# Performance work log

Measured on AMD Instinct MI355X. Metric: run time of the kernel, lower is better.

## Reference

```python
import jax, jax.numpy as jnp
import numpy as np

N_QUBITS = 4
N_LAYERS = 2
BATCH = 524288


def _ry(theta):
    # RY(theta) = [[cos(t/2), -sin(t/2)], [sin(t/2), cos(t/2)]], shape [..., 2, 2]
    c = jnp.cos(theta / 2)
    s = jnp.sin(theta / 2)
    return jnp.stack([jnp.stack([c, -s], -1), jnp.stack([s, c], -1)], -2).astype(jnp.complex64)


def _rz(theta):
    # RZ(theta) = diag(exp(-i t/2), exp(i t/2))
    p = jnp.exp(-1j * theta / 2)
    pc = jnp.exp(1j * theta / 2)
    z = jnp.zeros_like(p)
    return jnp.stack([jnp.stack([p, z], -1), jnp.stack([z, pc], -1)], -2).astype(jnp.complex64)


def _apply_1q(state, gate, q):
    # state: [B,2,2,2,2] (axis 1+q is qubit q, wire 0 most significant as in default.qubit)
    # gate: [2,2] (shared) or [B,2,2] (per-sample)
    letters = list('abcd')
    t = letters[q]
    out = letters.copy()
    out[q] = 'z'
    if gate.ndim == 3:
        sub = f"Bz{t},B{''.join(letters)}->B{''.join(out)}"
    else:
        sub = f"z{t},B{''.join(letters)}->B{''.join(out)}"
    return jnp.einsum(sub, gate, state)


def _cnot(state, c, t):
    # flip target axis on the control=1 slice
    s0 = jnp.take(state, 0, axis=1 + c)
    s1 = jnp.take(state, 1, axis=1 + c)
    ta = 1 + t - (1 if t > c else 0)
    s1 = jnp.flip(s1, axis=ta)
    return jnp.stack([s0, s1], axis=1 + c)


def _circuit(x, weights):
    B = x.shape[0]
    state = jnp.zeros((B, 2, 2, 2, 2), jnp.complex64).at[:, 0, 0, 0, 0].set(1.0)
    ry_in = _ry(x)  # [B, 4, 2, 2], per-sample input encoding
    for q in range(N_QUBITS):
        state = _apply_1q(state, ry_in[:, q], q)
    for l in range(N_LAYERS):
        for q in range(N_QUBITS):
            state = _apply_1q(state, _rz(weights[l, q, 0]), q)
            state = _apply_1q(state, _ry(weights[l, q, 1]), q)
        for q in range(N_QUBITS - 1):
            state = _cnot(state, q, q + 1)
        state = _cnot(state, N_QUBITS - 1, 0)
    probs = jnp.abs(state.reshape(B, 16)) ** 2
    # <Z_i> = sum_s p(s) * (1 - 2*bit_i(s)); wire 0 is the most significant bit
    bits = (np.arange(16)[:, None] >> np.arange(N_QUBITS - 1, -1, -1)) & 1
    signs = jnp.asarray(1.0 - 2.0 * bits, jnp.float32)  # [16, 4]
    return probs @ signs  # [B, 4]


def setup_inputs() -> dict:
    key = jax.random.key(0)
    k1, k2 = jax.random.split(key)
    x = jax.random.normal(k1, (BATCH, N_QUBITS), dtype=jnp.float32)
    # TorchLayer default init: uniform in [0, 2*pi)
    weights = jax.random.uniform(k2, (N_LAYERS, N_QUBITS, 2), dtype=jnp.float32, minval=0.0, maxval=2 * np.pi)
    return {"x": x, "weights": weights}


def reference(x, weights):
    return _circuit(x, weights)
```

## Files before the change

kernel.cpp:

```cpp
#include <hip/hip_runtime.h>

#define BATCH 524288
#define TPB 256
#define V 2

__global__ void qprep_kernel(const float* __restrict__ w, float* __restrict__ ws) {
    const int tid = threadIdx.x;
    if (tid >= 16) return;

    float stx[16], sty[16];
    #pragma unroll
    for (int i = 0; i < 16; i++) { stx[i] = 0.f; sty[i] = 0.f; }
    stx[tid] = 1.f;

    #pragma unroll
    for (int l = 0; l < 2; l++) {
        #pragma unroll
        for (int q = 0; q < 4; q++) {
            float cz, sz, cy, sy;
            __sincosf(0.5f * w[l * 8 + q * 2 + 0], &sz, &cz);
            __sincosf(0.5f * w[l * 8 + q * 2 + 1], &sy, &cy);
            const int mask = 8 >> q;
            #pragma unroll
            for (int i = 0; i < 16; i++) {
                float ax = stx[i], ay = sty[i];
                if (i & mask) { stx[i] = ax * cz - ay * sz; sty[i] = ay * cz + ax * sz; }
                else          { stx[i] = ax * cz + ay * sz; sty[i] = ay * cz - ax * sz; }
            }
            #pragma unroll
            for (int i = 0; i < 16; i++) {
                if (!(i & mask)) {
                    float a0x = stx[i], a0y = sty[i];
                    float a1x = stx[i | mask], a1y = sty[i | mask];
                    stx[i]        = cy * a0x - sy * a1x;
                    sty[i]        = cy * a0y - sy * a1y;
                    stx[i | mask] = sy * a0x + cy * a1x;
                    sty[i | mask] = sy * a0y + cy * a1y;
                }
            }
        }
        #pragma unroll
        for (int e = 0; e < 4; e++) {
            const int cqs[4] = {0, 1, 2, 3};
            const int tqs[4] = {1, 2, 3, 0};
            const int cm = 8 >> cqs[e];
            const int tm = 8 >> tqs[e];
            #pragma unroll
            for (int i = 0; i < 16; i++) {
                if ((i & cm) && !(i & tm)) {
                    float t0x = stx[i], t0y = sty[i];
                    stx[i] = stx[i | tm]; sty[i] = sty[i | tm];
                    stx[i | tm] = t0x;    sty[i | tm] = t0y;
                }
            }
        }
    }
    #pragma unroll
    for (int j = 0; j < 16; j++) {
        ws[j * 32 + tid]      = stx[j];
        ws[j * 32 + 16 + tid] = sty[j];
    }
}

__global__ __launch_bounds__(TPB, 4) void qmain_kernel(const float* __restrict__ x,
                                                       const float* __restrict__ U,
                                                       float* __restrict__ out) {
    const int base = blockIdx.x * (TPB * V) + threadIdx.x;

    float sv[V][16];
    #pragma unroll
    for (int v = 0; v < V; v++) {
        const int smp = base + v * TPB;
        const float4 xv = reinterpret_cast<const float4*>(x)[smp];
        float c0, s0, c1, s1, c2, s2, c3, s3;
        __sincosf(0.5f * xv.x, &s0, &c0);
        __sincosf(0.5f * xv.y, &s1, &c1);
        __sincosf(0.5f * xv.z, &s2, &c2);
        __sincosf(0.5f * xv.w, &s3, &c3);
        const float p01[4] = {c0 * c1, c0 * s1, s0 * c1, s0 * s1};
        const float p23[4] = {c2 * c3, c2 * s3, s2 * c3, s2 * s3};
        #pragma unroll
        for (int i = 0; i < 16; i++) sv[v][i] = p01[i >> 2] * p23[i & 3];
    }

    float z[V][4];
    #pragma unroll
    for (int v = 0; v < V; v++)
        #pragma unroll
        for (int i = 0; i < 4; i++) z[v][i] = 0.f;

    #pragma unroll
    for (int j = 0; j < 16; j++) {
        float re[V], im[V];
        #pragma unroll
        for (int v = 0; v < V; v++) { re[v] = 0.f; im[v] = 0.f; }
        #pragma unroll
        for (int k = 0; k < 16; k++) {
            const float ur = U[j * 32 + k];
            const float ui = U[j * 32 + 16 + k];
            #pragma unroll
            for (int v = 0; v < V; v++) {
                re[v] = fmaf(ur, sv[v][k], re[v]);
                im[v] = fmaf(ui, sv[v][k], im[v]);
            }
        }
        #pragma unroll
        for (int v = 0; v < V; v++) {
            const float p = re[v] * re[v] + im[v] * im[v];
            z[v][0] += (j & 8) ? -p : p;
            z[v][1] += (j & 4) ? -p : p;
            z[v][2] += (j & 2) ? -p : p;
            z[v][3] += (j & 1) ? -p : p;
        }
    }

    #pragma unroll
    for (int v = 0; v < V; v++) {
        const int smp = base + v * TPB;
        reinterpret_cast<float4*>(out)[smp] = make_float4(z[v][0], z[v][1], z[v][2], z[v][3]);
    }
}

extern "C" void kernel_launch(void* const* d_in, const int* in_sizes, int n_in,
                              void* d_out, int out_size, void* d_ws, size_t ws_size,
                              hipStream_t stream) {
    const float* x = (const float*)d_in[0];
    const float* w = (const float*)d_in[1];
    float* out = (float*)d_out;
    float* U = (float*)d_ws;

    qprep_kernel<<<1, 64, 0, stream>>>(w, U);
    const int grid = BATCH / (TPB * V);
    qmain_kernel<<<grid, TPB, 0, stream>>>(x, U, out);
}
```

Before: 68.79 us.

## Fuse unitary prep into main kernel via shared memory and skip basis state zero

The separate single-thread-block prep kernel is removed. Each block now rebuilds the 16x16 circuit unitary in shared memory with 16 threads, then synchronises before the batch work. The main loop reads unitary rows as float4 from LDS instead of global memory. Because the state is normalised, it skips basis state 0 and derives each <Z_i> as 1-2*sum of probabilities with bit i set. This cuts one kernel launch and one sixteenth of the matvec work, but every block now repeats the prep serially, and the result relies on the norm being exactly 1.

```diff
diff --git a/kernel.cpp b/kernel.cpp
--- a/kernel.cpp
+++ b/kernel.cpp
@@ -4,68 +4,69 @@
 #define TPB 256
 #define V 2
 
-__global__ void qprep_kernel(const float* __restrict__ w, float* __restrict__ ws) {
+__global__ __launch_bounds__(TPB, 4) void qfused_kernel(const float* __restrict__ x,
+                                                        const float* __restrict__ w,
+                                                        float* __restrict__ out) {
+    __shared__ __align__(16) float Ush[512];
     const int tid = threadIdx.x;
-    if (tid >= 16) return;
 
-    float stx[16], sty[16];
-    #pragma unroll
-    for (int i = 0; i < 16; i++) { stx[i] = 0.f; sty[i] = 0.f; }
-    stx[tid] = 1.f;
+    if (tid < 16) {
+        float stx[16], sty[16];
+        #pragma unroll
+        for (int i = 0; i < 16; i++) { stx[i] = 0.f; sty[i] = 0.f; }
+        stx[tid] = 1.f;
 
-    #pragma unroll
-    for (int l = 0; l < 2; l++) {
         #pragma unroll
-        for (int q = 0; q < 4; q++) {
-            float cz, sz, cy, sy;
-            __sincosf(0.5f * w[l * 8 + q * 2 + 0], &sz, &cz);
-            __sincosf(0.5f * w[l * 8 + q * 2 + 1], &sy, &cy);
-            const int mask = 8 >> q;
+        for (int l = 0; l < 2; l++) {
             #pragma unroll
-            for (int i = 0; i < 16; i++) {
-                float ax = stx[i], ay = sty[i];
-                if (i & mask) { stx[i] = ax * cz - ay * sz; sty[i] = ay * cz + ax * sz; }
-                else          { stx[i] = ax * cz + ay * sz; sty[i] = ay * cz - ax * sz; }
+            for (int q = 0; q < 4; q++) {
+                float cz, sz, cy, sy;
+                __sincosf(0.5f * w[l * 8 + q * 2 + 0], &sz, &cz);
+                __sincosf(0.5f * w[l * 8 + q * 2 + 1], &sy, &cy);
+                const int mask = 8 >> q;
+                #pragma unroll
+                for (int i = 0; i < 16; i++) {
+                    float ax = stx[i], ay = sty[i];
+                    if (i & mask) { stx[i] = ax * cz - ay * sz; sty[i] = ay * cz + ax * sz; }
+                    else          { stx[i] = ax * cz + ay * sz; sty[i] = ay * cz - ax * sz; }
+                }
+                #pragma unroll
+                for (int i = 0; i < 16; i++) {
+                    if (!(i & mask)) {
+                        float a0x = stx[i], a0y = sty[i];
+                        float a1x = stx[i | mask], a1y = sty[i | mask];
+                        stx[i]        = cy * a0x - sy * a1x;
+                        sty[i]        = cy * a0y - sy * a1y;
+                        stx[i | mask] = sy * a0x + cy * a1x;
+                        sty[i | mask] = sy * a0y + cy * a1y;
+                    }
+                }
             }
             #pragma unroll
-            for (int i = 0; i < 16; i++) {
-                if (!(i & mask)) {
-                    float a0x = stx[i], a0y = sty[i];
-                    float a1x = stx[i | mask], a1y = sty[i | mask];
-                    stx[i]        = cy * a0x - sy * a1x;
-                    sty[i]        = cy * a0y - sy * a1y;
-                    stx[i | mask] = sy * a0x + cy * a1x;
-                    sty[i | mask] = sy * a0y + cy * a1y;
+            for (int e = 0; e < 4; e++) {
+                const int cqs[4] = {0, 1, 2, 3};
+                const int tqs[4] = {1, 2, 3, 0};
+                const int cm = 8 >> cqs[e];
+                const int tm = 8 >> tqs[e];
+                #pragma unroll
+                for (int i = 0; i < 16; i++) {
+                    if ((i & cm) && !(i & tm)) {
+                        float t0x = stx[i], t0y = sty[i];
+                        stx[i] = stx[i | tm]; sty[i] = sty[i | tm];
+                        stx[i | tm] = t0x;    sty[i | tm] = t0y;
+                    }
                 }
             }
         }
         #pragma unroll
-        for (int e = 0; e < 4; e++) {
-            const int cqs[4] = {0, 1, 2, 3};
-            const int tqs[4] = {1, 2, 3, 0};
-            const int cm = 8 >> cqs[e];
-            const int tm = 8 >> tqs[e];
-            #pragma unroll
-            for (int i = 0; i < 16; i++) {
-                if ((i & cm) && !(i & tm)) {
-                    float t0x = stx[i], t0y = sty[i];
-                    stx[i] = stx[i | tm]; sty[i] = sty[i | tm];
-                    stx[i | tm] = t0x;    sty[i | tm] = t0y;
-                }
-            }
+        for (int j = 0; j < 16; j++) {
+            Ush[j * 32 + tid]      = stx[j];
+            Ush[j * 32 + 16 + tid] = sty[j];
         }
     }
-    #pragma unroll
-    for (int j = 0; j < 16; j++) {
-        ws[j * 32 + tid]      = stx[j];
-        ws[j * 32 + 16 + tid] = sty[j];
-    }
-}
+    __syncthreads();
 
-__global__ __launch_bounds__(TPB, 4) void qmain_kernel(const float* __restrict__ x,
-                                                       const float* __restrict__ U,
-                                                       float* __restrict__ out) {
-    const int base = blockIdx.x * (TPB * V) + threadIdx.x;
+    const int base = blockIdx.x * (TPB * V) + tid;
 
     float sv[V][16];
     #pragma unroll
@@ -83,41 +84,44 @@
         for (int i = 0; i < 16; i++) sv[v][i] = p01[i >> 2] * p23[i & 3];
     }
 
-    float z[V][4];
+    float acc[V][4];
     #pragma unroll
     for (int v = 0; v < V; v++)
         #pragma unroll
-        for (int i = 0; i < 4; i++) z[v][i] = 0.f;
+        for (int i = 0; i < 4; i++) acc[v][i] = 0.f;
 
     #pragma unroll
-    for (int j = 0; j < 16; j++) {
-        float re[V], im[V];
+    for (int j = 1; j < 16; j++) {
+        float ur[16], ui[16];
         #pragma unroll
-        for (int v = 0; v < V; v++) { re[v] = 0.f; im[v] = 0.f; }
-        #pragma unroll
-        for (int k = 0; k < 16; k++) {
-            const float ur = U[j * 32 + k];
-            const float ui = U[j * 32 + 16 + k];
-            #pragma unroll
-            for (int v = 0; v < V; v++) {
-                re[v] = fmaf(ur, sv[v][k], re[v]);
-                im[v] = fmaf(ui, sv[v][k], im[v]);
-            }
+        for (int t = 0; t < 4; t++) {
+            const float4 a = reinterpret_cast<const float4*>(Ush + j * 32)[t];
+            ur[4 * t + 0] = a.x; ur[4 * t + 1] = a.y; ur[4 * t + 2] = a.z; ur[4 * t + 3] = a.w;
+            const float4 b = reinterpret_cast<const float4*>(Ush + j * 32 + 16)[t];
+            ui[4 * t + 0] = b.x; ui[4 * t + 1] = b.y; ui[4 * t + 2] = b.z; ui[4 * t + 3] = b.w;
         }
         #pragma unroll
         for (int v = 0; v < V; v++) {
-            const float p = re[v] * re[v] + im[v] * im[v];
-            z[v][0] += (j & 8) ? -p : p;
-            z[v][1] += (j & 4) ? -p : p;
-            z[v][2] += (j & 2) ? -p : p;
-            z[v][3] += (j & 1) ? -p : p;
+            float re = 0.f, im = 0.f;
+            #pragma unroll
+            for (int k = 0; k < 16; k++) {
+                re = fmaf(ur[k], sv[v][k], re);
+                im = fmaf(ui[k], sv[v][k], im);
+            }
+            const float p = fmaf(re, re, im * im);
+            if (j & 8) acc[v][0] += p;
+            if (j & 4) acc[v][1] += p;
+            if (j & 2) acc[v][2] += p;
+            if (j & 1) acc[v][3] += p;
         }
     }
 
     #pragma unroll
     for (int v = 0; v < V; v++) {
         const int smp = base + v * TPB;
-        reinterpret_cast<float4*>(out)[smp] = make_float4(z[v][0], z[v][1], z[v][2], z[v][3]);
+        reinterpret_cast<float4*>(out)[smp] =
+            make_float4(fmaf(-2.f, acc[v][0], 1.f), fmaf(-2.f, acc[v][1], 1.f),
+                        fmaf(-2.f, acc[v][2], 1.f), fmaf(-2.f, acc[v][3], 1.f));
     }
 }
 
@@ -127,9 +131,6 @@
     const float* x = (const float*)d_in[0];
     const float* w = (const float*)d_in[1];
     float* out = (float*)d_out;
-    float* U = (float*)d_ws;
-
-    qprep_kernel<<<1, 64, 0, stream>>>(w, U);
     const int grid = BATCH / (TPB * V);
-    qmain_kernel<<<grid, TPB, 0, stream>>>(x, U, out);
+    qfused_kernel<<<grid, TPB, 0, stream>>>(x, w, out);
 }
```

Result: slower. 94.41 us (+37.2%).

## Compute circuit unitary product with split-fp16 MFMA instead of scalar FMAs

Applied to the files above, without the earlier changes.

The per-sample 16x16 complex unitary times real state vector is moved onto MFMA 16x16x32 f16 instructions. Both the unitary and the state are split into high and low fp16 parts to recover near-fp32 accuracy. The state vectors are staged through swizzled shared memory, and the Z expectations are reduced with cross-lane shuffles. One sample per thread replaces two, which adds an LDS round trip and a block barrier in exchange for removing the large scalar FMA count.

```diff
diff --git a/kernel.cpp b/kernel.cpp
--- a/kernel.cpp
+++ b/kernel.cpp
@@ -2,7 +2,9 @@
 
 #define BATCH 524288
 #define TPB 256
-#define V 2
+
+typedef _Float16 half8 __attribute__((ext_vector_type(8)));
+typedef float f32x4 __attribute__((ext_vector_type(4)));
 
 __global__ void qprep_kernel(const float* __restrict__ w, float* __restrict__ ws) {
     const int tid = threadIdx.x;
@@ -65,59 +67,93 @@
 __global__ __launch_bounds__(TPB, 4) void qmain_kernel(const float* __restrict__ x,
                                                        const float* __restrict__ U,
                                                        float* __restrict__ out) {
-    const int base = blockIdx.x * (TPB * V) + threadIdx.x;
+    __shared__ __align__(16) _Float16 Sb[TPB * 32];
 
-    float sv[V][16];
+    const int tid  = threadIdx.x;
+    const int lane = tid & 63;
+    const int wave = tid >> 6;
+    const int l15  = lane & 15;
+    const int lg   = lane >> 4;
+
+    const int k8 = (lg & 1) * 8;
+    const float* urow = U + l15 * 32 + k8;
+    const float4 r0 = *reinterpret_cast<const float4*>(urow);
+    const float4 r1 = *reinterpret_cast<const float4*>(urow + 4);
+    const float4 i0 = *reinterpret_cast<const float4*>(urow + 16);
+    const float4 i1 = *reinterpret_cast<const float4*>(urow + 20);
+    const float ur[8] = {r0.x, r0.y, r0.z, r0.w, r1.x, r1.y, r1.z, r1.w};
+    const float ui[8] = {i0.x, i0.y, i0.z, i0.w, i1.x, i1.y, i1.z, i1.w};
+    half8 a_rh, a_rl, a_ih, a_il;
     #pragma unroll
-    for (int v = 0; v < V; v++) {
-        const int smp = base + v * TPB;
-        const float4 xv = reinterpret_cast<const float4*>(x)[smp];
-        float c0, s0, c1, s1, c2, s2, c3, s3;
-        __sincosf(0.5f * xv.x, &s0, &c0);
-        __sincosf(0.5f * xv.y, &s1, &c1);
-        __sincosf(0.5f * xv.z, &s2, &c2);
-        __sincosf(0.5f * xv.w, &s3, &c3);
-        const float p01[4] = {c0 * c1, c0 * s1, s0 * c1, s0 * s1};
-        const float p23[4] = {c2 * c3, c2 * s3, s2 * c3, s2 * s3};
-        #pragma unroll
-        for (int i = 0; i < 16; i++) sv[v][i] = p01[i >> 2] * p23[i & 3];
+    for (int i = 0; i < 8; i++) {
+        const _Float16 h = (_Float16)ur[i];
+        a_rh[i] = h;
+        a_rl[i] = (_Float16)(ur[i] - (float)h);
+        const _Float16 g = (_Float16)ui[i];
+        a_ih[i] = g;
+        a_il[i] = (_Float16)(ui[i] - (float)g);
     }
 
-    float z[V][4];
+    const int samp = blockIdx.x * TPB + tid;
+    const float4 xv = reinterpret_cast<const float4*>(x)[samp];
+    float c0, s0, c1, s1, c2, s2, c3, s3;
+    __sincosf(0.5f * xv.x, &s0, &c0);
+    __sincosf(0.5f * xv.y, &s1, &c1);
+    __sincosf(0.5f * xv.z, &s2, &c2);
+    __sincosf(0.5f * xv.w, &s3, &c3);
+    const float p01[4] = {c0 * c1, c0 * s1, s0 * c1, s0 * s1};
+    const float p23[4] = {c2 * c3, c2 * s3, s2 * c3, s2 * s3};
+    half8 ch[4];
     #pragma unroll
-    for (int v = 0; v < V; v++)
+    for (int i = 0; i < 16; i++) {
+        const float sv = p01[i >> 2] * p23[i & 3];
+        const _Float16 h = (_Float16)sv;
+        ch[i >> 3][i & 7]       = h;
+        ch[2 + (i >> 3)][i & 7] = (_Float16)(sv - (float)h);
+    }
+    {
+        _Float16* rowp = Sb + tid * 32;
+        const int swz = (tid >> 1) & 3;
         #pragma unroll
-        for (int i = 0; i < 4; i++) z[v][i] = 0.f;
+        for (int c = 0; c < 4; c++)
+            *reinterpret_cast<half8*>(rowp + ((c ^ swz) * 8)) = ch[c];
+    }
+    __syncthreads();
+
+    const int rs = lg ^ ((l15 >> 1) & 3);
+    const _Float16* rp = Sb + (wave * 64 + l15) * 32 + rs * 8;
+    const int obase = blockIdx.x * TPB + wave * 64;
 
     #pragma unroll
-    for (int j = 0; j < 16; j++) {
-        float re[V], im[V];
-        #pragma unroll
-        for (int v = 0; v < V; v++) { re[v] = 0.f; im[v] = 0.f; }
-        #pragma unroll
-        for (int k = 0; k < 16; k++) {
-            const float ur = U[j * 32 + k];
-            const float ui = U[j * 32 + 16 + k];
-            #pragma unroll
-            for (int v = 0; v < V; v++) {
-                re[v] = fmaf(ur, sv[v][k], re[v]);
-                im[v] = fmaf(ui, sv[v][k], im[v]);
-            }
-        }
-        #pragma unroll
-        for (int v = 0; v < V; v++) {
-            const float p = re[v] * re[v] + im[v] * im[v];
-            z[v][0] += (j & 8) ? -p : p;
-            z[v][1] += (j & 4) ? -p : p;
-            z[v][2] += (j & 2) ? -p : p;
-            z[v][3] += (j & 1) ? -p : p;
-        }
-    }
+    for (int T = 0; T < 4; T++) {
+        const half8 b = *reinterpret_cast<const half8*>(rp + T * 512);
+        f32x4 cre = {0.f, 0.f, 0.f, 0.f}, cim = {0.f, 0.f, 0.f, 0.f};
+        cre = __builtin_amdgcn_mfma_f32_16x16x32_f16(a_rh, b, cre, 0, 0, 0);
+        cre = __builtin_amdgcn_mfma_f32_16x16x32_f16(a_rl, b, cre, 0, 0, 0);
+        cim = __builtin_amdgcn_mfma_f32_16x16x32_f16(a_ih, b, cim, 0, 0, 0);
+        cim = __builtin_amdgcn_mfma_f32_16x16x32_f16(a_il, b, cim, 0, 0, 0);
 
-    #pragma unroll
-    for (int v = 0; v < V; v++) {
-        const int smp = base + v * TPB;
-        reinterpret_cast<float4*>(out)[smp] = make_float4(z[v][0], z[v][1], z[v][2], z[v][3]);
+        const float q0 = fmaf(cre[0], cre[0], cim[0] * cim[0]);
+        const float q1 = fmaf(cre[1], cre[1], cim[1] * cim[1]);
+        const float q2 = fmaf(cre[2], cre[2], cim[2] * cim[2]);
+        const float q3 = fmaf(cre[3], cre[3], cim[3] * cim[3]);
+        const float s01 = q0 + q1, s23 = q2 + q3;
+        const float t = s01 + s23;
+        const float u = s01 - s23;
+        const float v = (q0 - q1) + (q2 - q3);
+        const float tx = __shfl_xor(t, 16);
+        const float t1 = t + tx;
+        const float z1 = t - tx;
+        const float u1 = u + __shfl_xor(u, 16);
+        const float v1 = v + __shfl_xor(v, 16);
+        const float z0  = t1 - __shfl_xor(t1, 32);
+        const float z1f = z1 + __shfl_xor(z1, 32);
+        const float z2  = u1 + __shfl_xor(u1, 32);
+        const float z3  = v1 + __shfl_xor(v1, 32);
+
+        if (lane < 16)
+            reinterpret_cast<float4*>(out)[obase + T * 16 + l15] =
+                make_float4(z0, z1f, z2, z3);
     }
 }
 
@@ -130,6 +166,6 @@
     float* U = (float*)d_ws;
 
     qprep_kernel<<<1, 64, 0, stream>>>(w, U);
-    const int grid = BATCH / (TPB * V);
+    const int grid = BATCH / TPB;
     qmain_kernel<<<grid, TPB, 0, stream>>>(x, U, out);
 }
```

New measurement: 69.55 us. About the same (+1.1%).
